# Kernel optimization log

Measured on AMD Instinct MI355X. Metric: run time of the kernel, lower is better.

## Reference

```python
import jax, jax.numpy as jnp
import numpy as np

T, B, LAG, H = 128, 1024, 6, 256


def setup_inputs() -> dict:
    key = jax.random.key(0)
    ks = jax.random.split(key, 16)
    s = 0.05  # small init scale to keep LSTM gates in a sane range
    d = {}
    d["x"] = jax.random.normal(ks[0], (T, B, LAG), jnp.float32)
    d["Wi1"] = jax.random.normal(ks[1], (H, LAG), jnp.float32) * s
    d["bi1"] = jnp.zeros((H,), jnp.float32)
    d["Wi2"] = jax.random.normal(ks[2], (H, H), jnp.float32) * s
    d["bi2"] = jnp.zeros((H,), jnp.float32)
    d["Wi3"] = jax.random.normal(ks[3], (H, H), jnp.float32) * s
    d["bi3"] = jnp.zeros((H,), jnp.float32)
    d["Wih0"] = jax.random.normal(ks[4], (4 * H, H), jnp.float32) * s
    d["Whh0"] = jax.random.normal(ks[5], (4 * H, H), jnp.float32) * s
    d["bih0"] = jnp.zeros((4 * H,), jnp.float32)
    d["bhh0"] = jnp.zeros((4 * H,), jnp.float32)
    d["Wih1"] = jax.random.normal(ks[6], (4 * H, H), jnp.float32) * s
    d["Whh1"] = jax.random.normal(ks[7], (4 * H, H), jnp.float32) * s
    d["bih1"] = jnp.zeros((4 * H,), jnp.float32)
    d["bhh1"] = jnp.zeros((4 * H,), jnp.float32)
    d["Wo1"] = jax.random.normal(ks[8], (H, H), jnp.float32) * s
    d["bo1"] = jnp.zeros((H,), jnp.float32)
    d["Wo2"] = jax.random.normal(ks[9], (H, H), jnp.float32) * s
    d["bo2"] = jnp.zeros((H,), jnp.float32)
    d["Wo3"] = jax.random.normal(ks[10], (LAG, H), jnp.float32) * s
    d["bo3"] = jnp.zeros((LAG,), jnp.float32)
    return d


def _lstm_cell(xt, h, c, Wih, Whh, bih, bhh):
    # PyTorch gate order: i, f, g, o
    g = xt @ Wih.T + h @ Whh.T + (bih + bhh)
    i, f, gg, o = jnp.split(g, 4, axis=-1)
    c2 = jax.nn.sigmoid(f) * c + jax.nn.sigmoid(i) * jnp.tanh(gg)
    h2 = jax.nn.sigmoid(o) * jnp.tanh(c2)
    return h2, c2


def reference(x, Wi1, bi1, Wi2, bi2, Wi3, bi3,
              Wih0, Whh0, bih0, bhh0, Wih1, Whh1, bih1, bhh1,
              Wo1, bo1, Wo2, bo2, Wo3, bo3):
    relu = jax.nn.relu
    # input MLP applied to every timestep at once: [T,B,6] -> [T,B,H]
    u = relu(x @ Wi1.T + bi1)
    u = relu(u @ Wi2.T + bi2)
    u = relu(u @ Wi3.T + bi3)

    def step(carry, xt):
        h0, c0, h1, c1 = carry
        h0, c0 = _lstm_cell(xt, h0, c0, Wih0, Whh0, bih0, bhh0)
        # dropout(0.05) between layers is identity in eval mode
        h1, c1 = _lstm_cell(h0, h1, c1, Wih1, Whh1, bih1, bhh1)
        return (h0, c0, h1, c1), h1

    z = jnp.zeros((x.shape[1], Whh0.shape[1]), x.dtype)
    _, hs = jax.lax.scan(step, (z, z, z, z), u)  # hs: [T,B,H]

    # output MLP: ReLU, Linear, ReLU, Linear, ReLU, Linear(H->6)
    y = relu(hs)
    y = relu(y @ Wo1.T + bo1)
    y = relu(y @ Wo2.T + bo2)
    y = y @ Wo3.T + bo3
    return y  # [T,B,6]
```

## Files before the change

kernel.cpp:

```cpp
#include <hip/hip_runtime.h>
#include <math.h>


namespace {
constexpr int kT   = 128;
constexpr int kB   = 1024;
constexpr int kLag = 6;
constexpr int kH   = 256;
constexpr int kTc  = 32;
constexpr int kMc  = kTc * kB;
constexpr int kGS  = 67;
constexpr int kLdsForce = 98304;
}

typedef _Float16 half8 __attribute__((ext_vector_type(8)));
typedef _Float16 half2 __attribute__((ext_vector_type(2)));
typedef float f32x4 __attribute__((ext_vector_type(4)));
typedef unsigned long long u64;

__device__ __forceinline__ float sigm(float x) {
    return 1.f / (1.f + exp2f(-1.4426950408889634f * x));
}
__device__ __forceinline__ float tanh_(float x) {
    return 2.f / (1.f + exp2f(-2.8853900817779268f * x)) - 1.f;
}

__device__ __forceinline__ half8 pack(u64 a, u64 b) {
    union { u64 u[2]; half8 h; } r;
    r.u[0] = a; r.u[1] = b;
    return r.h;
}

__device__ __forceinline__ void ld_l2(half8& d, const _Float16* p) {
    asm volatile("global_load_dwordx4 %0, %1, off sc0"
                 : "=v"(d) : "v"(p) : "memory");
}
__device__ __forceinline__ void ld_pln(half8& d, const _Float16* p) {
    asm volatile("global_load_dwordx4 %0, %1, off"
                 : "=v"(d) : "v"(p) : "memory");
}
#define WAITCNT_HOLD16(A)                                                     \
    asm volatile("s_waitcnt vmcnt(0)"                                         \
        : "+v"(A[0]), "+v"(A[1]), "+v"(A[2]), "+v"(A[3]),                     \
          "+v"(A[4]), "+v"(A[5]), "+v"(A[6]), "+v"(A[7]),                     \
          "+v"(A[8]), "+v"(A[9]), "+v"(A[10]), "+v"(A[11]),                   \
          "+v"(A[12]), "+v"(A[13]), "+v"(A[14]), "+v"(A[15]))

__global__ __launch_bounds__(256)
void zero_fill(unsigned int* __restrict__ p)
{
    p[blockIdx.x * 256 + threadIdx.x] = 0u;
}

__global__ __launch_bounds__(256)
void cvt_f2h(const float* __restrict__ s, _Float16* __restrict__ d)
{
    const int i = blockIdx.x * 256 + threadIdx.x;
    d[i] = (_Float16)s[i];
}

__global__ __launch_bounds__(256)
void build_wcat(const float* __restrict__ Wih, const float* __restrict__ Whh,
                _Float16* __restrict__ d)
{
    const int i = blockIdx.x * 256 + threadIdx.x;
    const int row = i >> 9, col = i & 511;
    const float v = (col < 256) ? Wih[row * 256 + col] : Whh[row * 256 + col - 256];
    d[i] = (_Float16)v;
}

__global__ __launch_bounds__(256)
void add_bias(const float* __restrict__ a, const float* __restrict__ b,
              float* __restrict__ d)
{
    const int i = blockIdx.x * 256 + threadIdx.x;
    d[i] = a[i] + b[i];
}

__global__ __launch_bounds__(256)
void in_mlp1(const float* __restrict__ x, const float* __restrict__ Wi1,
             const float* __restrict__ bi1, _Float16* __restrict__ out)
{
    const int idx = blockIdx.x * 256 + threadIdx.x;
    const int col = idx & (kH - 1);
    const int row = idx >> 8;
    const float* xr = x + (size_t)row * kLag;
    const float* w  = Wi1 + col * kLag;
    float s = bi1[col];
#pragma unroll
    for (int k = 0; k < kLag; ++k) s = fmaf(xr[k], w[k], s);
    out[idx] = (_Float16)fmaxf(s, 0.f);
}

__global__ __launch_bounds__(256)
void gemm_h16(const _Float16* __restrict__ A, const _Float16* __restrict__ W,
              const float* __restrict__ bias, _Float16* __restrict__ C)
{
    const int tid = threadIdx.x;
    const int w = tid >> 6, lane = tid & 63, q = lane >> 4, l15 = lane & 15;
    const int n0 = blockIdx.x * 64;
    const int r0 = blockIdx.y * 128 + w * 32;

    half8 bf[4][8];
#pragma unroll
    for (int nt = 0; nt < 4; ++nt)
#pragma unroll
        for (int kk = 0; kk < 8; ++kk)
            bf[nt][kk] = *(const half8*)(W + (size_t)(n0 + nt * 16 + l15) * 256
                                         + kk * 32 + q * 8);
    float bz[4];
#pragma unroll
    for (int nt = 0; nt < 4; ++nt) bz[nt] = bias[n0 + nt * 16 + l15];

#pragma unroll
    for (int rt = 0; rt < 2; ++rt) {
        const _Float16* arow = A + (size_t)(r0 + rt * 16 + l15) * 256 + q * 8;
        half8 af[8];
#pragma unroll
        for (int kk = 0; kk < 8; ++kk) af[kk] = *(const half8*)(arow + kk * 32);
        f32x4 acc[4];
#pragma unroll
        for (int nt = 0; nt < 4; ++nt)
            acc[nt] = (f32x4){bz[nt], bz[nt], bz[nt], bz[nt]};
#pragma unroll
        for (int kk = 0; kk < 8; ++kk)
#pragma unroll
            for (int nt = 0; nt < 4; ++nt)
                acc[nt] = __builtin_amdgcn_mfma_f32_16x16x32_f16(
                    af[kk], bf[nt][kk], acc[nt], 0, 0, 0);
#pragma unroll
        for (int nt = 0; nt < 4; ++nt)
#pragma unroll
            for (int r = 0; r < 4; ++r) {
                const float v = fmaxf(acc[nt][r], 0.f);
                C[(size_t)(r0 + rt * 16 + q * 4 + r) * 256 + n0 + nt * 16 + l15]
                    = (_Float16)v;
            }
    }
}

__device__ __forceinline__ void xbar(unsigned int* __restrict__ cptr,
                                     unsigned int target, int tid)
{
    asm volatile("s_waitcnt vmcnt(0)" ::: "memory");
    __syncthreads();
    if (tid == 0) {
        __hip_atomic_fetch_add(cptr, 1u, __ATOMIC_RELAXED,
                               __HIP_MEMORY_SCOPE_AGENT);
        while (__hip_atomic_load(cptr, __ATOMIC_RELAXED,
                                 __HIP_MEMORY_SCOPE_AGENT) < target)
            __builtin_amdgcn_s_sleep(1);
    }
    __syncthreads();
}

__device__ __forceinline__ void gather_lo(const _Float16* lo, int row, int q,
                                          u64* ua)
{
    const u64* plo = (const u64*)(lo + (size_t)row * 256 + q * 8);
#pragma unroll
    for (int kk = 0; kk < 8; ++kk) {
        ua[2*kk]   = plo[kk*8];
        ua[2*kk+1] = plo[kk*8 + 1];
    }
}

__device__ __forceinline__ void gstore(float* __restrict__ gl, int m0, int nb,
                                       int q, int l15,
                                       const f32x4& a0, const f32x4& a1)
{
#pragma unroll
    for (int r = 0; r < 4; ++r) {
        gl[(m0 + q*4 + r) * kGS + nb + l15]      = a0[r];
        gl[(m0 + q*4 + r) * kGS + nb + 16 + l15] = a1[r];
    }
}

template<bool CLO>
__device__ __forceinline__ void phase_gemm(
    const _Float16* __restrict__ lo, const _Float16* __restrict__ hi,
    const half8 (&B0)[16], const half8 (&B1)[16],
    float* __restrict__ gl, int rtb, int nb, int q, int l15)
{
#pragma unroll
    for (int rt = 0; rt < 2; ++rt) {
        const int row = (rtb + rt) * 16 + l15;
        const _Float16* plo = lo + (size_t)row * 256 + q * 8;
        const _Float16* phi = hi + (size_t)row * 256 + q * 8;
        half8 A[16];
#pragma unroll
        for (int kk = 0; kk < 8; ++kk) {
            if (CLO) ld_l2(A[kk], plo + kk * 32);
            else     ld_pln(A[kk], plo + kk * 32);
            ld_l2(A[8 + kk], phi + kk * 32);
        }
        WAITCNT_HOLD16(A);
        f32x4 a0 = {0.f,0.f,0.f,0.f}, a1 = {0.f,0.f,0.f,0.f};
#pragma unroll
        for (int kk = 0; kk < 16; ++kk) {
            a0 = __builtin_amdgcn_mfma_f32_16x16x32_f16(A[kk], B0[kk], a0, 0,0,0);
            a1 = __builtin_amdgcn_mfma_f32_16x16x32_f16(A[kk], B1[kk], a1, 0,0,0);
        }
        gstore(gl, (rtb + rt) * 16, nb, q, l15, a0, a1);
    }
}

__device__ __forceinline__ void cell_one(const float* __restrict__ gl,
    int crow, int cc, const float* __restrict__ bs, float* __restrict__ cst,
    _Float16* __restrict__ hout, _Float16* __restrict__ uout)
{
    const float* gr = gl + crow * kGS;
    _Float16 hp[2];
#pragma unroll
    for (int e = 0; e < 2; ++e) {
        const float gi = gr[0*16 + cc + e] + bs[e*4 + 0];
        const float gf = gr[1*16 + cc + e] + bs[e*4 + 1];
        const float gg = gr[2*16 + cc + e] + bs[e*4 + 2];
        const float go = gr[3*16 + cc + e] + bs[e*4 + 3];
        const float c2 = sigm(gf) * cst[e] + sigm(gi) * tanh_(gg);
        cst[e] = c2;
        hp[e] = (_Float16)(sigm(go) * tanh_(c2));
    }
    *(half2*)(hout + (size_t)crow * 256 + cc) = (half2){hp[0], hp[1]};
    if (uout) {
        const _Float16 z = (_Float16)0.f;
        *(half2*)(uout + (size_t)crow * 256 + cc) =
            (half2){hp[0] > z ? hp[0] : z, hp[1] > z ? hp[1] : z};
    }
}

__global__ __launch_bounds__(512, 2)
void lstm_all(_Float16* __restrict__ ubuf,
              const _Float16* __restrict__ Wc0, const _Float16* __restrict__ Wc1,
              const float* __restrict__ bc0, const float* __restrict__ bc1,
              _Float16* __restrict__ h0b, _Float16* __restrict__ h1b,
              unsigned int* __restrict__ cnt)
{
    extern __shared__ char lds[];
    float* gl0 = (float*)lds;
    float* gl1 = gl0 + 64 * kGS;

    const int tid = threadIdx.x;
    const int w = tid >> 6, lane = tid & 63, q = lane >> 4, l15 = lane & 15;
    const int wl = w & 3;
    const int rtb = (wl >> 1) * 2;
    const int nb  = (wl & 1) * 32;
    const int lyr = (w < 4) ? 1 : 0;

    __shared__ int sh_bi, sh_js;
    if (tid == 0) {
        unsigned int xcd = __builtin_amdgcn_s_getreg(20 | (31 << 11)) & 7u;
        unsigned int rank = __hip_atomic_fetch_add(cnt + 512 + xcd * 16, 1u,
            __ATOMIC_RELAXED, __HIP_MEMORY_SCOPE_AGENT);
        sh_bi = (int)(xcd * 2 + (rank >> 4));
        sh_js = (int)(rank & 15);
    }
    __syncthreads();
    const int bi = sh_bi, js = sh_js;
    unsigned int* cptr = cnt + bi * 32;

    const _Float16* WcL = lyr ? Wc1 : Wc0;
    half8 Bf0[16], Bf1[16];
    {
        const _Float16* wr0 = WcL
            + (size_t)((nb >> 4) * 256 + js * 16 + l15) * 512 + q * 8;
        const _Float16* wr1 = WcL
            + (size_t)(((nb >> 4) + 1) * 256 + js * 16 + l15) * 512 + q * 8;
#pragma unroll
        for (int kk = 0; kk < 16; ++kk) {
            Bf0[kk] = *(const half8*)(wr0 + kk * 32);
            Bf1[kk] = *(const half8*)(wr1 + kk * 32);
        }
    }

    const int cc = (tid & 7) * 2;
    const int crow = tid >> 3;
    float bs0[8], bs1[8];
#pragma unroll
    for (int e = 0; e < 2; ++e)
#pragma unroll
        for (int g = 0; g < 4; ++g) {
            bs0[e*4 + g] = bc0[g * 256 + js * 16 + cc + e];
            bs1[e*4 + g] = bc1[g * 256 + js * 16 + cc + e];
        }
    float cst0[2] = {0.f, 0.f}, cst1[2] = {0.f, 0.f};
    const size_t rbase = (size_t)bi * 64 * 256;
    const size_t obase = rbase + js * 16;

    if (lyr == 0) {
#pragma unroll
        for (int rt = 0; rt < 2; ++rt) {
            u64 ua[16];
            gather_lo(ubuf + rbase, (rtb + rt) * 16 + l15, q, ua);
            f32x4 a0 = {0.f,0.f,0.f,0.f}, a1 = {0.f,0.f,0.f,0.f};
#pragma unroll
            for (int kk = 0; kk < 8; ++kk) {
                const half8 af = pack(ua[2*kk], ua[2*kk+1]);
                a0 = __builtin_amdgcn_mfma_f32_16x16x32_f16(af, Bf0[kk], a0, 0,0,0);
                a1 = __builtin_amdgcn_mfma_f32_16x16x32_f16(af, Bf1[kk], a1, 0,0,0);
            }
            gstore(gl0, (rtb + rt) * 16, nb, q, l15, a0, a1);
        }
    }
    __syncthreads();
    cell_one(gl0, crow, cc, bs0, cst0, h0b + obase, nullptr);
    xbar(cptr, 16u, tid);

    for (int t = 0; t < kT; ++t) {
        const size_t p  = (size_t)(t & 1) * kB * 256;
        const size_t pn = (size_t)((t & 1) ^ 1) * kB * 256;
        const bool hasB = (t < kT - 1);
        if (lyr == 1) {
            phase_gemm<true>(h0b + p + rbase, h1b + pn + rbase,
                             Bf0, Bf1, gl1, rtb, nb, q, l15);
        } else if (hasB) {
            phase_gemm<false>(ubuf + (size_t)(t + 1) * kB * 256 + rbase,
                              h0b + p + rbase,
                              Bf0, Bf1, gl0, rtb, nb, q, l15);
        }
        __syncthreads();
        cell_one(gl1, crow, cc, bs1, cst1, h1b + p + obase,
                 ubuf + (size_t)t * kB * 256 + obase);
        if (hasB) {
            cell_one(gl0, crow, cc, bs0, cst0, h0b + pn + obase, nullptr);
            xbar(cptr, (unsigned)(16 * (t + 2)), tid);
        }
    }
}

__global__ __launch_bounds__(256)
void out_mlp3(const _Float16* __restrict__ y2, const float* __restrict__ Wo3,
              const float* __restrict__ bo3, float* __restrict__ out)
{
    const int lane = threadIdx.x & 63;
    const int row  = blockIdx.x * 4 + (threadIdx.x >> 6);
    const _Float16* yr = y2 + (size_t)row * kH + lane * 4;
    const float a0 = (float)yr[0], a1 = (float)yr[1], a2 = (float)yr[2], a3 = (float)yr[3];
    float s[kLag];
#pragma unroll
    for (int o = 0; o < kLag; ++o) {
        const float4 wv = *(const float4*)(Wo3 + o * kH + lane * 4);
        s[o] = a0 * wv.x + a1 * wv.y + a2 * wv.z + a3 * wv.w;
    }
#pragma unroll
    for (int off = 32; off > 0; off >>= 1) {
#pragma unroll
        for (int o = 0; o < kLag; ++o) s[o] += __shfl_down(s[o], off);
    }
    if (lane == 0) {
#pragma unroll
        for (int o = 0; o < kLag; ++o)
            out[(size_t)row * kLag + o] = s[o] + bo3[o];
    }
}

extern "C" void kernel_launch(void* const* d_in, const int* in_sizes, int n_in,
                              void* d_out, int out_size, void* d_ws, size_t ws_size,
                              hipStream_t stream)
{
    const float* x    = (const float*)d_in[0];
    const float* Wi1  = (const float*)d_in[1];
    const float* bi1  = (const float*)d_in[2];
    const float* Wi2  = (const float*)d_in[3];
    const float* bi2  = (const float*)d_in[4];
    const float* Wi3  = (const float*)d_in[5];
    const float* bi3  = (const float*)d_in[6];
    const float* Wih0 = (const float*)d_in[7];
    const float* Whh0 = (const float*)d_in[8];
    const float* bih0 = (const float*)d_in[9];
    const float* bhh0 = (const float*)d_in[10];
    const float* Wih1 = (const float*)d_in[11];
    const float* Whh1 = (const float*)d_in[12];
    const float* bih1 = (const float*)d_in[13];
    const float* bhh1 = (const float*)d_in[14];
    const float* Wo1  = (const float*)d_in[15];
    const float* bo1  = (const float*)d_in[16];
    const float* Wo2  = (const float*)d_in[17];
    const float* bo2  = (const float*)d_in[18];
    const float* Wo3  = (const float*)d_in[19];
    const float* bo3  = (const float*)d_in[20];
    float* outp = (float*)d_out;

    char* p = (char*)d_ws;
    _Float16* ubuf = (_Float16*)p;  p += (size_t)kT * kB * kH * 2;
    _Float16* s1   = (_Float16*)p;  p += (size_t)kMc * kH * 2;
    _Float16* s2   = (_Float16*)p;  p += (size_t)kMc * kH * 2;
    _Float16* Wc0  = (_Float16*)p;  p += (size_t)1024 * 512 * 2;
    _Float16* Wc1  = (_Float16*)p;  p += (size_t)1024 * 512 * 2;
    _Float16* W2h  = (_Float16*)p;  p += (size_t)kH * kH * 2;
    _Float16* W3h  = (_Float16*)p;  p += (size_t)kH * kH * 2;
    _Float16* Wo1h = (_Float16*)p;  p += (size_t)kH * kH * 2;
    _Float16* Wo2h = (_Float16*)p;  p += (size_t)kH * kH * 2;
    float* bc0 = (float*)p;  p += 1024 * 4;
    float* bc1 = (float*)p;  p += 1024 * 4;
    _Float16* h0b = (_Float16*)p;  p += (size_t)2 * kB * kH * 2;
    _Float16* h1b = (_Float16*)p;  p += (size_t)2 * kB * kH * 2;
    unsigned int* cnt = (unsigned int*)p;  p += 4096;

    zero_fill<<<2052, 256, 0, stream>>>((unsigned int*)h0b);
    cvt_f2h<<<kH * kH / 256, 256, 0, stream>>>(Wi2, W2h);
    cvt_f2h<<<kH * kH / 256, 256, 0, stream>>>(Wi3, W3h);
    cvt_f2h<<<kH * kH / 256, 256, 0, stream>>>(Wo1, Wo1h);
    cvt_f2h<<<kH * kH / 256, 256, 0, stream>>>(Wo2, Wo2h);
    build_wcat<<<1024 * 512 / 256, 256, 0, stream>>>(Wih0, Whh0, Wc0);
    build_wcat<<<1024 * 512 / 256, 256, 0, stream>>>(Wih1, Whh1, Wc1);
    add_bias<<<4, 256, 0, stream>>>(bih0, bhh0, bc0);
    add_bias<<<4, 256, 0, stream>>>(bih1, bhh1, bc1);

    for (int c = 0; c < kT / kTc; ++c) {
        in_mlp1<<<kMc * kH / 256, 256, 0, stream>>>(
            x + (size_t)c * kMc * kLag, Wi1, bi1, s1);
        gemm_h16<<<dim3(4, kMc / 128), 256, 0, stream>>>(s1, W2h, bi2, s2);
        gemm_h16<<<dim3(4, kMc / 128), 256, 0, stream>>>(
            s2, W3h, bi3, ubuf + (size_t)c * kMc * kH);
    }

    static bool attr_set = false;
    if (!attr_set) {
        hipFuncSetAttribute((const void*)lstm_all,
                            hipFuncAttributeMaxDynamicSharedMemorySize, kLdsForce);
        attr_set = true;
    }
    void* args[] = {&ubuf, &Wc0, &Wc1, &bc0, &bc1, &h0b, &h1b, &cnt};
    hipLaunchCooperativeKernel((const void*)lstm_all, dim3(256), dim3(512),
                               args, kLdsForce, stream);

    for (int c = 0; c < kT / kTc; ++c) {
        gemm_h16<<<dim3(4, kMc / 128), 256, 0, stream>>>(
            ubuf + (size_t)c * kMc * kH, Wo1h, bo1, s1);
        gemm_h16<<<dim3(4, kMc / 128), 256, 0, stream>>>(s1, Wo2h, bo2, s2);
        out_mlp3<<<kMc / 4, 256, 0, stream>>>(
            s2, Wo3, bo3, outp + (size_t)c * kMc * kLag);
    }
}
```

Before: 1.965 ms.

## Stage recurrent h tiles in swizzled LDS once per step instead of per-wave global loads

After: 1.993 ms. Within noise of the previous version (+1.4%).

```diff
diff --git a/kernel.cpp b/kernel.cpp
--- a/kernel.cpp
+++ b/kernel.cpp
@@ -10,7 +10,7 @@
 constexpr int kTc  = 32;
 constexpr int kMc  = kTc * kB;
 constexpr int kGS  = 67;
-constexpr int kLdsForce = 98304;
+constexpr int kLdsBytes = 2 * 32768 + 2 * 64 * kGS * 4;
 }
 
 typedef _Float16 half8 __attribute__((ext_vector_type(8)));
@@ -35,16 +35,10 @@
     asm volatile("global_load_dwordx4 %0, %1, off sc0"
                  : "=v"(d) : "v"(p) : "memory");
 }
-__device__ __forceinline__ void ld_pln(half8& d, const _Float16* p) {
-    asm volatile("global_load_dwordx4 %0, %1, off"
-                 : "=v"(d) : "v"(p) : "memory");
-}
-#define WAITCNT_HOLD16(A)                                                     \
+#define WAITCNT_HOLD8(A, B)                                                   \
     asm volatile("s_waitcnt vmcnt(0)"                                         \
         : "+v"(A[0]), "+v"(A[1]), "+v"(A[2]), "+v"(A[3]),                     \
-          "+v"(A[4]), "+v"(A[5]), "+v"(A[6]), "+v"(A[7]),                     \
-          "+v"(A[8]), "+v"(A[9]), "+v"(A[10]), "+v"(A[11]),                   \
-          "+v"(A[12]), "+v"(A[13]), "+v"(A[14]), "+v"(A[15]))
+          "+v"(B[0]), "+v"(B[1]), "+v"(B[2]), "+v"(B[3]))
 
 __global__ __launch_bounds__(256)
 void zero_fill(unsigned int* __restrict__ p)
@@ -176,30 +170,54 @@
     }
 }
 
-template<bool CLO>
-__device__ __forceinline__ void phase_gemm(
-    const _Float16* __restrict__ lo, const _Float16* __restrict__ hi,
+__device__ __forceinline__ void phase_gemm_lds2(
+    const char* pA, const char* pB,
     const half8 (&B0)[16], const half8 (&B1)[16],
     float* __restrict__ gl, int rtb, int nb, int q, int l15)
 {
 #pragma unroll
     for (int rt = 0; rt < 2; ++rt) {
         const int row = (rtb + rt) * 16 + l15;
-        const _Float16* plo = lo + (size_t)row * 256 + q * 8;
-        const _Float16* phi = hi + (size_t)row * 256 + q * 8;
-        half8 A[16];
+        const int xr  = ((row & 15) << 4) ^ ((row & 1) << 8);
+        const int rb  = row * 512;
+        f32x4 a0 = {0.f,0.f,0.f,0.f}, a1 = {0.f,0.f,0.f,0.f};
 #pragma unroll
         for (int kk = 0; kk < 8; ++kk) {
-            if (CLO) ld_l2(A[kk], plo + kk * 32);
-            else     ld_pln(A[kk], plo + kk * 32);
-            ld_l2(A[8 + kk], phi + kk * 32);
-        }
-        WAITCNT_HOLD16(A);
+            const int off = rb + ((q * 16 + kk * 64) ^ xr);
+            const half8 alo = *(const half8*)(pA + off);
+            const half8 ahi = *(const half8*)(pB + off);
+            a0 = __builtin_amdgcn_mfma_f32_16x16x32_f16(alo, B0[kk],     a0, 0,0,0);
+            a1 = __builtin_amdgcn_mfma_f32_16x16x32_f16(alo, B1[kk],     a1, 0,0,0);
+            a0 = __builtin_amdgcn_mfma_f32_16x16x32_f16(ahi, B0[8 + kk], a0, 0,0,0);
+            a1 = __builtin_amdgcn_mfma_f32_16x16x32_f16(ahi, B1[8 + kk], a1, 0,0,0);
+        }
+        gstore(gl, (rtb + rt) * 16, nb, q, l15, a0, a1);
+    }
+}
+
+__device__ __forceinline__ void phase_gemm_l0(
+    const _Float16* __restrict__ u, const char* pH0,
+    const half8 (&B0)[16], const half8 (&B1)[16],
+    float* __restrict__ gl, int rtb, int nb, int q, int l15)
+{
+#pragma unroll
+    for (int rt = 0; rt < 2; ++rt) {
+        const int row = (rtb + rt) * 16 + l15;
+        const int xr  = ((row & 15) << 4) ^ ((row & 1) << 8);
+        const int rb  = row * 512;
+        const _Float16* pu = u + (size_t)row * 256 + q * 8;
+        half8 uf[8];
+#pragma unroll
+        for (int kk = 0; kk < 8; ++kk) uf[kk] = *(const half8*)(pu + kk * 32);
         f32x4 a0 = {0.f,0.f,0.f,0.f}, a1 = {0.f,0.f,0.f,0.f};
 #pragma unroll
-        for (int kk = 0; kk < 16; ++kk) {
-            a0 = __builtin_amdgcn_mfma_f32_16x16x32_f16(A[kk], B0[kk], a0, 0,0,0);
-            a1 = __builtin_amdgcn_mfma_f32_16x16x32_f16(A[kk], B1[kk], a1, 0,0,0);
+        for (int kk = 0; kk < 8; ++kk) {
+            const int off = rb + ((q * 16 + kk * 64) ^ xr);
+            const half8 ah = *(const half8*)(pH0 + off);
+            a0 = __builtin_amdgcn_mfma_f32_16x16x32_f16(uf[kk], B0[kk],   a0, 0,0,0);
+            a1 = __builtin_amdgcn_mfma_f32_16x16x32_f16(uf[kk], B1[kk],   a1, 0,0,0);
+            a0 = __builtin_amdgcn_mfma_f32_16x16x32_f16(ah, B0[8 + kk],   a0, 0,0,0);
+            a1 = __builtin_amdgcn_mfma_f32_16x16x32_f16(ah, B1[8 + kk],   a1, 0,0,0);
         }
         gstore(gl, (rtb + rt) * 16, nb, q, l15, a0, a1);
     }
@@ -237,7 +255,9 @@
               unsigned int* __restrict__ cnt)
 {
     extern __shared__ char lds[];
-    float* gl0 = (float*)lds;
+    char* pH0  = lds;
+    char* pH1  = lds + 32768;
+    float* gl0 = (float*)(lds + 65536);
     float* gl1 = gl0 + 64 * kGS;
 
     const int tid = threadIdx.x;
@@ -273,6 +293,15 @@
         }
     }
 
+    int sdst[4];
+#pragma unroll
+    for (int r = 0; r < 4; ++r) {
+        const int L   = tid * 16 + r * 8192;
+        const int row = L >> 9;
+        const int c   = L & 511;
+        sdst[r] = row * 512 + (c ^ ((row & 15) << 4) ^ ((row & 1) << 8));
+    }
+
     const int cc = (tid & 7) * 2;
     const int crow = tid >> 3;
     float bs0[8], bs1[8];
@@ -310,15 +339,33 @@
         const size_t p  = (size_t)(t & 1) * kB * 256;
         const size_t pn = (size_t)((t & 1) ^ 1) * kB * 256;
         const bool hasB = (t < kT - 1);
+
+        {
+            half8 s0[4], s1h[4];
+            const char* b0 = (const char*)(h0b + p  + rbase);
+            const char* b1 = (const char*)(h1b + pn + rbase);
+#pragma unroll
+            for (int r = 0; r < 4; ++r) {
+                ld_l2(s0[r],  (const _Float16*)(b0 + tid * 16 + r * 8192));
+                ld_l2(s1h[r], (const _Float16*)(b1 + tid * 16 + r * 8192));
+            }
+            WAITCNT_HOLD8(s0, s1h);
+#pragma unroll
+            for (int r = 0; r < 4; ++r) {
+                *(half8*)(pH0 + sdst[r]) = s0[r];
+                *(half8*)(pH1 + sdst[r]) = s1h[r];
+            }
+        }
+        __syncthreads();
+
         if (lyr == 1) {
-            phase_gemm<true>(h0b + p + rbase, h1b + pn + rbase,
-                             Bf0, Bf1, gl1, rtb, nb, q, l15);
+            phase_gemm_lds2(pH0, pH1, Bf0, Bf1, gl1, rtb, nb, q, l15);
         } else if (hasB) {
-            phase_gemm<false>(ubuf + (size_t)(t + 1) * kB * 256 + rbase,
-                              h0b + p + rbase,
-                              Bf0, Bf1, gl0, rtb, nb, q, l15);
+            phase_gemm_l0(ubuf + (size_t)(t + 1) * kB * 256 + rbase, pH0,
+                          Bf0, Bf1, gl0, rtb, nb, q, l15);
         }
         __syncthreads();
+
         cell_one(gl1, crow, cc, bs1, cst1, h1b + p + obase,
                  ubuf + (size_t)t * kB * 256 + obase);
         if (hasB) {
@@ -418,12 +465,12 @@
     static bool attr_set = false;
     if (!attr_set) {
         hipFuncSetAttribute((const void*)lstm_all,
-                            hipFuncAttributeMaxDynamicSharedMemorySize, kLdsForce);
+                            hipFuncAttributeMaxDynamicSharedMemorySize, kLdsBytes);
         attr_set = true;
     }
     void* args[] = {&ubuf, &Wc0, &Wc1, &bc0, &bc1, &h0b, &h1b, &cnt};
     hipLaunchCooperativeKernel((const void*)lstm_all, dim3(256), dim3(512),
-                               args, kLdsForce, stream);
+                               args, kLdsBytes, stream);
 
     for (int c = 0; c < kT / kTc; ++c) {
         gemm_h16<<<dim3(4, kMc / 128), 256, 0, stream>>>(
```
